# Performance work log

Hardware: AMD Instinct MI355X
Metric: run time of the kernel (lower is better)

The kernel has to match this reference:

```python
import jax, jax.numpy as jnp
import numpy as np

N_NODES = 100000
N_EDGES = 1600000
IN_CH = 128
TYPE_EMB = 32
OUT_CH = 128
N_REL = 8
N_BASES = 8
N_NTYPES = 8
FEAT = IN_CH + TYPE_EMB  # 160, RGCNConv input dim after concat


def setup_inputs() -> dict:
    key = jax.random.key(0)
    ks = jax.random.split(key, 9)
    x = jax.random.normal(ks[0], (N_NODES, IN_CH), dtype=jnp.float32)
    node_type_ids = jax.random.randint(ks[1], (N_NODES,), 0, N_NTYPES)
    edge_index = jax.random.randint(ks[2], (2, N_EDGES), 0, N_NODES)
    edge_type = jax.random.randint(ks[3], (N_EDGES,), 0, N_REL)
    emb_table = jax.random.normal(ks[4], (N_NTYPES, TYPE_EMB), dtype=jnp.float32)
    bases = jax.random.normal(ks[5], (N_BASES, FEAT, OUT_CH), dtype=jnp.float32) * (1.0 / np.sqrt(FEAT))
    comp = jax.random.normal(ks[6], (N_REL, N_BASES), dtype=jnp.float32) * (1.0 / np.sqrt(N_BASES))
    root_w = jax.random.normal(ks[7], (FEAT, OUT_CH), dtype=jnp.float32) * (1.0 / np.sqrt(FEAT))
    bias = jnp.zeros((OUT_CH,), dtype=jnp.float32)
    return {"x": x, "node_type_ids": node_type_ids, "edge_index": edge_index,
            "edge_type": edge_type, "emb_table": emb_table, "bases": bases,
            "comp": comp, "root_w": root_w, "bias": bias}


def reference(x, node_type_ids, edge_index, edge_type, emb_table, bases, comp, root_w, bias):
    N = x.shape[0]
    # node-type embedding lookup + concat
    h = jnp.concatenate([x, emb_table[node_type_ids]], axis=1)  # [N, FEAT]
    # basis decomposition: per-relation weights [R, FEAT, OUT]
    weight = jnp.einsum('rb,bio->rio', comp, bases)
    src, dst = edge_index[0], edge_index[1]
    h_src = h[src]  # [E, FEAT] -- dominant gather
    # root/self transform + bias
    out = h @ root_w + bias
    # PyG RGCNConv default aggr='mean': per-relation mean over incoming edges, summed across relations
    for r in range(weight.shape[0]):
        m = (edge_type == r).astype(h.dtype)  # [E]
        s = jax.ops.segment_sum(h_src * m[:, None], dst, num_segments=N)  # [N, FEAT]
        c = jax.ops.segment_sum(m, dst, num_segments=N)                    # [N]
        mean_r = s / jnp.maximum(c, 1.0)[:, None]
        out = out + mean_r @ weight[r]
    # dropout is identity in eval mode
    return jax.nn.relu(out)
```

## Files before the change

kernel.cpp:

```cpp
#include <hip/hip_runtime.h>

#define NN 100000
#define NE 1600000
#define INC 128
#define TE 32
#define OC 128
#define NR 8
#define NBASES 8
#define FT 160
#define KP 168
#define KW 160
#define TN 32
#define NBKT 3125
#define NCH 256
#define EPB 6250
#define CAP 896

typedef float f32x4 __attribute__((ext_vector_type(4)));
typedef float f32x2 __attribute__((ext_vector_type(2)));
typedef __bf16 bf16x8 __attribute__((ext_vector_type(8)));

__device__ __forceinline__ unsigned f2bf1(float f) {
    unsigned u = __float_as_uint(f);
    return (u + 0x7fffu + ((u >> 16) & 1u)) >> 16;
}

__device__ __forceinline__ float bflo(unsigned u) { return __uint_as_float(u << 16); }
__device__ __forceinline__ float bfhi(unsigned u) { return __uint_as_float(u & 0xFFFF0000u); }

__device__ __forceinline__ unsigned cvtpk(float a, float b) {
    unsigned r;
    asm("v_cvt_pk_bf16_f32 %0, %1, %2" : "=v"(r) : "v"(a), "v"(b));
    return r;
}

__device__ __forceinline__ int bscan_excl(int v, int* tmp) {
    int tid = threadIdx.x;
    tmp[tid] = v; __syncthreads();
#pragma unroll
    for (int d = 1; d < 256; d <<= 1) {
        int t = (tid >= d) ? tmp[tid - d] : 0;
        __syncthreads();
        tmp[tid] += t;
        __syncthreads();
    }
    return tmp[tid] - v;
}

__global__ __launch_bounds__(256) void k_prep(
    const float* __restrict__ x, const int* __restrict__ nt,
    const float* __restrict__ emb, const float* __restrict__ comp,
    const float* __restrict__ bases, const float* __restrict__ rootw,
    const int* __restrict__ ei,
    unsigned short* __restrict__ h, unsigned short* __restrict__ Wt,
    int* __restrict__ ghist, int* __restrict__ total) {
    __shared__ int hist[NBKT];
    int tid = threadIdx.x;
    int b = blockIdx.x;
    if (b < NCH) {
        for (int j = tid; j < NBKT; j += 256) hist[j] = 0;
        __syncthreads();
        int e0 = b * EPB;
#pragma unroll
        for (int kk = 0; kk < 28; kk += 4) {
            int dv[4];
#pragma unroll
            for (int u = 0; u < 4; u++) {
                int i = (kk + u) * 256 + tid;
                dv[u] = (i < EPB) ? ei[NE + e0 + i] : -1;
            }
#pragma unroll
            for (int u = 0; u < 4; u++)
                if (dv[u] >= 0) atomicAdd(&hist[dv[u] >> 5], 1);
        }
        __syncthreads();
        int* g = ghist + (size_t)b * NBKT;
        for (int j = tid; j < NBKT; j += 256) {
            int v = hist[j];
            g[j] = v;
            if (v) atomicAdd(&total[j], v);
        }
        return;
    }
    int idx = (b - NCH) * 256 + tid;
    if (idx < 9 * 128 * KW) {
        int ridx = idx / (128 * KW);
        int rem  = idx % (128 * KW);
        int o = rem / KW;
        int k = rem % KW;
        float v = 0.f;
        if (k < 128) {
            if (ridx < NR) {
#pragma unroll
                for (int bb = 0; bb < NBASES; bb++)
                    v += comp[ridx * NBASES + bb] * bases[(bb * FT + k) * OC + o];
            } else {
                v = rootw[k * OC + o];
            }
        } else if (k < 136) {
            int t = k - 128;
            if (ridx < NR) {
#pragma unroll
                for (int bb = 0; bb < NBASES; bb++) {
                    float cb = comp[ridx * NBASES + bb], s2 = 0.f;
                    for (int k2 = 0; k2 < TE; k2++)
                        s2 += emb[t * TE + k2] * bases[(bb * FT + 128 + k2) * OC + o];
                    v += cb * s2;
                }
            } else {
                for (int k2 = 0; k2 < TE; k2++)
                    v += emb[t * TE + k2] * rootw[(128 + k2) * OC + o];
            }
        }
        Wt[idx] = (unsigned short)f2bf1(v);
    }
    if (idx < NN * 16) {
        int n = idx / 16, c = idx % 16;
        const float* p = x + (size_t)n * INC + c * 8;
        f32x4 v0 = *(const f32x4*)p, v1 = *(const f32x4*)(p + 4);
        uint4 o;
        o.x = f2bf1(v0.x) | (f2bf1(v0.y) << 16);
        o.y = f2bf1(v0.z) | (f2bf1(v0.w) << 16);
        o.z = f2bf1(v1.x) | (f2bf1(v1.y) << 16);
        o.w = f2bf1(v1.z) | (f2bf1(v1.w) << 16);
        *(uint4*)(h + (size_t)n * INC + c * 8) = o;
    }
}

__global__ __launch_bounds__(256) void k_scan(const int* __restrict__ total,
                                              int* __restrict__ bstart) {
    __shared__ int tmp[256];
    int tid = threadIdx.x, s = 0, i0 = tid * 13;
    int loc[13];
#pragma unroll
    for (int i = 0; i < 13; i++) {
        int j = i0 + i;
        loc[i] = (j < NBKT) ? total[j] : 0;
        s += loc[i];
    }
    int run = bscan_excl(s, tmp);
#pragma unroll
    for (int i = 0; i < 13; i++) {
        int j = i0 + i;
        if (j < NBKT) { bstart[j] = run; run += loc[i]; }
    }
    if (tid == 0) bstart[NBKT] = NE;
}

__global__ __launch_bounds__(256) void k_off(int* __restrict__ ghist,
                                             const int* __restrict__ bstart) {
    int w = (blockIdx.x * 256 + threadIdx.x) >> 6;
    int lane = threadIdx.x & 63;
    if (w >= NBKT) return;
    size_t base = (size_t)(lane * 4) * NBKT + w;
    int v[4];
#pragma unroll
    for (int k = 0; k < 4; k++) v[k] = ghist[base + (size_t)k * NBKT];
    int s = v[0] + v[1] + v[2] + v[3];
    int inc = s;
#pragma unroll
    for (int d = 1; d < 64; d <<= 1) {
        int t = __shfl_up(inc, d, 64);
        if (lane >= d) inc += t;
    }
    int run = bstart[w] + inc - s;
#pragma unroll
    for (int k = 0; k < 4; k++) {
        ghist[base + (size_t)k * NBKT] = run;
        run += v[k];
    }
}

__global__ __launch_bounds__(256) void k_scatter(const int* __restrict__ ei, const int* __restrict__ et,
                                                 const int* __restrict__ nt,
                                                 const int* __restrict__ ghist, unsigned* __restrict__ slots) {
    __shared__ int cur[NBKT];
    int tid = threadIdx.x, b = blockIdx.x;
    for (int j = tid; j < NBKT; j += 256) cur[j] = ghist[(size_t)b * NBKT + j];
    __syncthreads();
    int e0 = b * EPB;
#pragma unroll
    for (int kk = 0; kk < 28; kk += 4) {
        int sv[4], dv[4], rv[4], tv[4];
#pragma unroll
        for (int u = 0; u < 4; u++) {
            int i = (kk + u) * 256 + tid;
            int e = e0 + ((i < EPB) ? i : 0);
            sv[u] = ei[e]; dv[u] = ei[NE + e]; rv[u] = et[e];
            if (i >= EPB) dv[u] = -1;
        }
#pragma unroll
        for (int u = 0; u < 4; u++) tv[u] = nt[sv[u]];
#pragma unroll
        for (int u = 0; u < 4; u++) {
            if (dv[u] >= 0) {
                int pos = atomicAdd(&cur[dv[u] >> 5], 1);
                slots[pos] = (unsigned)sv[u] | ((unsigned)rv[u] << 17)
                           | ((unsigned)(dv[u] & 31) << 20) | ((unsigned)tv[u] << 25);
            }
        }
    }
}

__global__ __launch_bounds__(256, 6) void k_mega(
    const unsigned short* __restrict__ h, const int* __restrict__ nt,
    const float* __restrict__ bias,
    const unsigned short* __restrict__ Wt, const int* __restrict__ bstart,
    const unsigned* __restrict__ slots, float* __restrict__ out) {
    __shared__ unsigned short featmem[2][TN * KP];
    __shared__ unsigned sl[CAP];
    __shared__ unsigned pkl[256];

    const int tid = threadIdx.x;
    const int lane = tid & 63;
    const int wave = tid >> 6;
    const int j = blockIdx.x;
    const int n0 = j * TN;

    unsigned* sl_in = reinterpret_cast<unsigned*>(&featmem[0][0]);
    int* hist = reinterpret_cast<int*>(&featmem[0][0]) + CAP;
    int* tmp  = reinterpret_cast<int*>(&featmem[0][0]) + CAP + 256;

    int s0 = bstart[j];
    int m = bstart[j + 1] - s0; if (m > CAP) m = CAP;
    for (int i = tid; i < m; i += 256) sl_in[i] = slots[s0 + i];
    hist[tid] = 0;
    __syncthreads();
    for (int i = tid; i < m; i += 256) {
        unsigned v = sl_in[i];
        atomicAdd(&hist[((v >> 17) & 7u) * 32u + ((v >> 20) & 31u)], 1);
    }
    __syncthreads();
    int v0 = hist[tid];
    int ex = bscan_excl(v0, tmp);
    pkl[tid] = (unsigned)ex | ((unsigned)v0 << 16);
    hist[tid] = ex;
    __syncthreads();
    for (int i = tid; i < m; i += 256) {
        unsigned v = sl_in[i];
        int p = atomicAdd(&hist[((v >> 17) & 7u) * 32u + ((v >> 20) & 31u)], 1);
        sl[p] = (v & 0x1FFFFu) | (((v >> 25) & 7u) << 17);
    }
    __syncthreads();

    for (int i = tid; i < TN * 20; i += 256) {
        int nl = i / 20, c = i % 20, n = n0 + nl;
        uint4 v;
        if (c < 16) {
            v = *reinterpret_cast<const uint4*>(h + (size_t)n * INC + c * 8);
        } else if (c == 16) {
            int t = nt[n];
            v.x = (t == 0 ? 0x3F80u : 0u) | (t == 1 ? 0x3F800000u : 0u);
            v.y = (t == 2 ? 0x3F80u : 0u) | (t == 3 ? 0x3F800000u : 0u);
            v.z = (t == 4 ? 0x3F80u : 0u) | (t == 5 ? 0x3F800000u : 0u);
            v.w = (t == 6 ? 0x3F80u : 0u) | (t == 7 ? 0x3F800000u : 0u);
        } else {
            v = (uint4){0u, 0u, 0u, 0u};
        }
        *reinterpret_cast<uint4*>(&featmem[0][nl * KP + c * 8]) = v;
    }

    f32x4 acc[4];
#pragma unroll
    for (int t = 0; t < 4; t++) acc[t] = (f32x4){0.f, 0.f, 0.f, 0.f};

    auto mfma_pass = [&](int ridx, const unsigned short* fm) {
        const unsigned short* fA = fm + (lane & 15) * KP + ((lane >> 4) * 8);
        const unsigned short* gB = Wt + (size_t)ridx * 128 * KW
                                   + (wave * 32 + (lane & 15)) * KW + ((lane >> 4) * 8);
#pragma unroll
        for (int kc = 0; kc < 5; kc++) {
            bf16x8 a0 = *reinterpret_cast<const bf16x8*>(fA + 0 * 16 * KP + kc * 32);
            bf16x8 a1 = *reinterpret_cast<const bf16x8*>(fA + 1 * 16 * KP + kc * 32);
#pragma unroll
            for (int ct = 0; ct < 2; ct++) {
                bf16x8 b = *reinterpret_cast<const bf16x8*>(gB + ct * 16 * KW + kc * 32);
                acc[0 * 2 + ct] = __builtin_amdgcn_mfma_f32_16x16x32_bf16(a0, b, acc[0 * 2 + ct], 0, 0, 0);
                acc[1 * 2 + ct] = __builtin_amdgcn_mfma_f32_16x16x32_bf16(a1, b, acc[1 * 2 + ct], 0, 0, 0);
            }
        }
    };

    const int g = tid >> 4, l = tid & 15;
    const unsigned* hw = reinterpret_cast<const unsigned*>(h);

    auto agg_pass = [&](int r, unsigned short* fm) {
        int b0 = r * 32 + 2 * g;
        unsigned pk0 = pkl[b0], pk1 = pkl[b0 + 1];
        int sbeg = (int)(pk0 & 0xffffu);
        int e1 = (int)(pk1 & 0xffffu);
        int send = e1 + (int)(pk1 >> 16);
        f32x2 sa[4];
#pragma unroll
        for (int i = 0; i < 4; i++) sa[i] = (f32x2){0.f, 0.f};
        f32x2 cnt2 = (f32x2){0.f, 0.f};
        float run = 0.f;
        for (int e = sbeg; e < send; e += 4) {
            uint2 wa[4], wb[4]; unsigned tpk = 0;
#pragma unroll
            for (int u = 0; u < 4; u++) {
                int eu = e + u; if (eu >= send) eu = send - 1;
                unsigned v = sl[eu];
                const unsigned* hp = hw + (size_t)(v & 0x1FFFFu) * 64 + 2 * l;
                wa[u] = *reinterpret_cast<const uint2*>(hp);
                wb[u] = *reinterpret_cast<const uint2*>(hp + 32);
                tpk |= ((v >> 17) & 7u) << (3 * u);
            }
#pragma unroll
            for (int u = 0; u < 4; u++) {
                if (e + u < send) {
                    sa[0] += (f32x2){bflo(wa[u].x), bfhi(wa[u].x)};
                    sa[1] += (f32x2){bflo(wa[u].y), bfhi(wa[u].y)};
                    sa[2] += (f32x2){bflo(wb[u].x), bfhi(wb[u].x)};
                    sa[3] += (f32x2){bflo(wb[u].y), bfhi(wb[u].y)};
                    int tt = (int)((tpk >> (3 * u)) & 7u);
                    cnt2.x += (tt == 2 * l)     ? 1.f : 0.f;
                    cnt2.y += (tt == 2 * l + 1) ? 1.f : 0.f;
                    run += 1.f;
                    int nx = e + u + 1;
                    if (nx == e1 || nx == send) {
                        int q = (e + u >= e1) ? 1 : 0;
                        float inv = __builtin_amdgcn_rcpf(run);
                        f32x2 m0 = sa[0] * inv, m1 = sa[1] * inv, m2 = sa[2] * inv,
                              m3 = sa[3] * inv, fr = cnt2 * inv;
                        unsigned* fp = reinterpret_cast<unsigned*>(fm + (2 * g + q) * KP);
                        uint2 oa, ob;
                        oa.x = cvtpk(m0.x, m0.y);
                        oa.y = cvtpk(m1.x, m1.y);
                        ob.x = cvtpk(m2.x, m2.y);
                        ob.y = cvtpk(m3.x, m3.y);
                        *reinterpret_cast<uint2*>(fp + 2 * l) = oa;
                        *reinterpret_cast<uint2*>(fp + 32 + 2 * l) = ob;
                        fp[64 + l] = cvtpk(fr.x, fr.y);
#pragma unroll
                        for (int i = 0; i < 4; i++) sa[i] = (f32x2){0.f, 0.f};
                        cnt2 = (f32x2){0.f, 0.f};
                        run = 0.f;
                    }
                }
            }
        }
#pragma unroll
        for (int q = 0; q < 2; q++) {
            if ((pkl[b0 + q] >> 16) == 0u) {
                unsigned* fp = reinterpret_cast<unsigned*>(fm + (2 * g + q) * KP);
                *reinterpret_cast<uint2*>(fp + 2 * l) = (uint2){0u, 0u};
                *reinterpret_cast<uint2*>(fp + 32 + 2 * l) = (uint2){0u, 0u};
                fp[64 + l] = 0u;
            }
        }
    };

    __syncthreads();
    int prev = 8;
    for (int r = 0; r < NR; r++) {
        agg_pass(r, &featmem[(r + 1) & 1][0]);
        mfma_pass(prev, &featmem[r & 1][0]);
        prev = r;
        __syncthreads();
    }
    mfma_pass(7, &featmem[0][0]);

    const int rq = lane >> 4;
#pragma unroll
    for (int ct = 0; ct < 2; ct++) {
        int col = wave * 32 + ct * 16 + (lane & 15);
        float bv = bias[col];
#pragma unroll
        for (int rt = 0; rt < 2; rt++) {
#pragma unroll
            for (int i = 0; i < 4; i++) {
                int n = n0 + rt * 16 + rq * 4 + i;
                float v = acc[rt * 2 + ct][i] + bv;
                out[(size_t)n * OC + col] = v > 0.f ? v : 0.f;
            }
        }
    }
}

extern "C" void kernel_launch(void* const* d_in, const int* in_sizes, int n_in,
                              void* d_out, int out_size, void* d_ws, size_t ws_size,
                              hipStream_t stream) {
    const float* x     = (const float*)d_in[0];
    const int*   ntype = (const int*)d_in[1];
    const int*   ei    = (const int*)d_in[2];
    const int*   et    = (const int*)d_in[3];
    const float* emb   = (const float*)d_in[4];
    const float* bases = (const float*)d_in[5];
    const float* comp  = (const float*)d_in[6];
    const float* rootw = (const float*)d_in[7];
    const float* bias  = (const float*)d_in[8];
    float* out = (float*)d_out;

    char* ws = (char*)d_ws;
    unsigned short* Wt     = (unsigned short*)(ws);
    unsigned short* h      = (unsigned short*)(ws + 368640);
    int*            ghist  = (int*)(ws + 25968640);
    int*            total  = (int*)(ws + 29168640);
    int*            bstart = (int*)(ws + 29181184);
    unsigned*       slots  = (unsigned*)(ws + 29193728);

    hipMemsetAsync(total, 0, NBKT * sizeof(int), stream);
    k_prep   <<<NCH + 6250, 256, 0, stream>>>(x, ntype, emb, comp, bases, rootw, ei, h, Wt, ghist, total);
    k_scan   <<<1,    256, 0, stream>>>(total, bstart);
    k_off    <<<782,  256, 0, stream>>>(ghist, bstart);
    k_scatter<<<NCH,  256, 0, stream>>>(ei, et, ntype, ghist, slots);
    k_mega   <<<NBKT, 256, 0, stream>>>(h, ntype, bias, Wt, bstart, slots, out);
}
```

Baseline: 338.6 us.

## Assign eight destination rows per wave with software-pipelined double-buffered gathers

The aggregation pass is remapped: each wave now walks 8 consecutive destination segments, and each lane handles one dword (2 bf16 features), where before 16-lane groups handled 2 segments with 4 dwords per lane. Gathers of 8 edges are double-buffered: the next batch is issued before the current one is accumulated, to hide global-load latency. The intent is fewer, wider, coalesced row loads per edge and more loads in flight. In exchange each wave runs longer serial segment chains, boundary checks against seven edges cost more, and the prefetch reads up to 16 edges past the end (clamped to the last edge).

Result: slower. 454.9 us (+34.3%).

```diff
diff --git a/kernel.cpp b/kernel.cpp
--- a/kernel.cpp
+++ b/kernel.cpp
@@ -281,72 +281,77 @@
         }
     };
 
-    const int g = tid >> 4, l = tid & 15;
     const unsigned* hw = reinterpret_cast<const unsigned*>(h);
+    const int tl2 = 2 * lane;
 
     auto agg_pass = [&](int r, unsigned short* fm) {
-        int b0 = r * 32 + 2 * g;
-        unsigned pk0 = pkl[b0], pk1 = pkl[b0 + 1];
-        int sbeg = (int)(pk0 & 0xffffu);
-        int e1 = (int)(pk1 & 0xffffu);
-        int send = e1 + (int)(pk1 >> 16);
-        f32x2 sa[4];
-#pragma unroll
-        for (int i = 0; i < 4; i++) sa[i] = (f32x2){0.f, 0.f};
-        f32x2 cnt2 = (f32x2){0.f, 0.f};
+        int b0 = r * 32 + wave * 8;
+        int sbeg = (int)(pkl[b0] & 0xffffu);
+        int e1 = (int)(pkl[b0 + 1] & 0xffffu);
+        int e2 = (int)(pkl[b0 + 2] & 0xffffu);
+        int e3 = (int)(pkl[b0 + 3] & 0xffffu);
+        int e4 = (int)(pkl[b0 + 4] & 0xffffu);
+        int e5 = (int)(pkl[b0 + 5] & 0xffffu);
+        int e6 = (int)(pkl[b0 + 6] & 0xffffu);
+        unsigned pk7 = pkl[b0 + 7];
+        int e7 = (int)(pk7 & 0xffffu);
+        int send = e7 + (int)(pk7 >> 16);
+
+        f32x2 sa = (f32x2){0.f, 0.f}, cnt2 = (f32x2){0.f, 0.f};
         float run = 0.f;
-        for (int e = sbeg; e < send; e += 4) {
-            uint2 wa[4], wb[4]; unsigned tpk = 0;
-#pragma unroll
-            for (int u = 0; u < 4; u++) {
-                int eu = e + u; if (eu >= send) eu = send - 1;
+        unsigned wA[8], wB[8]; unsigned tA = 0, tB = 0;
+
+        auto issue = [&](int eb, unsigned* w, unsigned& tp) {
+            tp = 0;
+#pragma unroll
+            for (int u = 0; u < 8; u++) {
+                int eu = eb + u; if (eu >= send) eu = send - 1;
                 unsigned v = sl[eu];
-                const unsigned* hp = hw + (size_t)(v & 0x1FFFFu) * 64 + 2 * l;
-                wa[u] = *reinterpret_cast<const uint2*>(hp);
-                wb[u] = *reinterpret_cast<const uint2*>(hp + 32);
-                tpk |= ((v >> 17) & 7u) << (3 * u);
-            }
-#pragma unroll
-            for (int u = 0; u < 4; u++) {
-                if (e + u < send) {
-                    sa[0] += (f32x2){bflo(wa[u].x), bfhi(wa[u].x)};
-                    sa[1] += (f32x2){bflo(wa[u].y), bfhi(wa[u].y)};
-                    sa[2] += (f32x2){bflo(wb[u].x), bfhi(wb[u].x)};
-                    sa[3] += (f32x2){bflo(wb[u].y), bfhi(wb[u].y)};
-                    int tt = (int)((tpk >> (3 * u)) & 7u);
-                    cnt2.x += (tt == 2 * l)     ? 1.f : 0.f;
-                    cnt2.y += (tt == 2 * l + 1) ? 1.f : 0.f;
+                w[u] = hw[(size_t)(v & 0x1FFFFu) * 64 + lane];
+                tp |= ((v >> 17) & 7u) << (3 * u);
+            }
+        };
+        auto consume = [&](int eb, const unsigned* w, unsigned tp) {
+#pragma unroll
+            for (int u = 0; u < 8; u++) {
+                int p = eb + u;
+                if (p < send) {
+                    unsigned dw = w[u];
+                    sa += (f32x2){bflo(dw), bfhi(dw)};
+                    int tt = (int)((tp >> (3 * u)) & 7u);
+                    cnt2.x += (tt == tl2)     ? 1.f : 0.f;
+                    cnt2.y += (tt == tl2 + 1) ? 1.f : 0.f;
                     run += 1.f;
-                    int nx = e + u + 1;
-                    if (nx == e1 || nx == send) {
-                        int q = (e + u >= e1) ? 1 : 0;
+                    int nx = p + 1;
+                    if (nx == e1 || nx == e2 || nx == e3 || nx == e4 ||
+                        nx == e5 || nx == e6 || nx == e7 || nx == send) {
+                        int q = (p >= e1) + (p >= e2) + (p >= e3) + (p >= e4)
+                              + (p >= e5) + (p >= e6) + (p >= e7);
                         float inv = __builtin_amdgcn_rcpf(run);
-                        f32x2 m0 = sa[0] * inv, m1 = sa[1] * inv, m2 = sa[2] * inv,
-                              m3 = sa[3] * inv, fr = cnt2 * inv;
-                        unsigned* fp = reinterpret_cast<unsigned*>(fm + (2 * g + q) * KP);
-                        uint2 oa, ob;
-                        oa.x = cvtpk(m0.x, m0.y);
-                        oa.y = cvtpk(m1.x, m1.y);
-                        ob.x = cvtpk(m2.x, m2.y);
-                        ob.y = cvtpk(m3.x, m3.y);
-                        *reinterpret_cast<uint2*>(fp + 2 * l) = oa;
-                        *reinterpret_cast<uint2*>(fp + 32 + 2 * l) = ob;
-                        fp[64 + l] = cvtpk(fr.x, fr.y);
-#pragma unroll
-                        for (int i = 0; i < 4; i++) sa[i] = (f32x2){0.f, 0.f};
-                        cnt2 = (f32x2){0.f, 0.f};
-                        run = 0.f;
+                        unsigned* fp = reinterpret_cast<unsigned*>(fm + (wave * 8 + q) * KP);
+                        fp[lane] = cvtpk(sa.x * inv, sa.y * inv);
+                        if (lane < 16) fp[64 + lane] = cvtpk(cnt2.x * inv, cnt2.y * inv);
+                        sa = (f32x2){0.f, 0.f}; cnt2 = (f32x2){0.f, 0.f}; run = 0.f;
                     }
                 }
             }
-        }
-#pragma unroll
-        for (int q = 0; q < 2; q++) {
+        };
+
+        if (sbeg < send) {
+            issue(sbeg, wA, tA);
+            for (int e = sbeg; e < send; e += 16) {
+                issue(e + 8, wB, tB);
+                consume(e, wA, tA);
+                issue(e + 16, wA, tA);
+                consume(e + 8, wB, tB);
+            }
+        }
+#pragma unroll
+        for (int q = 0; q < 8; q++) {
             if ((pkl[b0 + q] >> 16) == 0u) {
-                unsigned* fp = reinterpret_cast<unsigned*>(fm + (2 * g + q) * KP);
-                *reinterpret_cast<uint2*>(fp + 2 * l) = (uint2){0u, 0u};
-                *reinterpret_cast<uint2*>(fp + 32 + 2 * l) = (uint2){0u, 0u};
-                fp[64 + l] = 0u;
+                unsigned* fp = reinterpret_cast<unsigned*>(fm + (wave * 8 + q) * KP);
+                fp[lane] = 0u;
+                if (lane < 16) fp[64 + lane] = 0u;
             }
         }
     };
```

## Fuse bucket scan and offset kernels into one grid-barrier kernel

Applied to the files above, without the earlier changes.

Replaces the single-block k_scan and the k_off kernel with one persistent kernel, k_sso. It computes the per-bucket totals from ghist, crosses a software grid barrier, has every block redundantly scan the totals in shared memory, then writes the per-chunk offsets. This removes the global atomicAdd into total inside k_prep, one kernel launch and the single-block serial scan stage. In exchange it adds a spin-wait grid barrier that assumes all 256 blocks are resident at once, and every block repeats the scan.

After: 393.9 us. 1.16x slower.

```diff
diff --git a/kernel.cpp b/kernel.cpp
--- a/kernel.cpp
+++ b/kernel.cpp
@@ -47,13 +47,28 @@
     return tmp[tid] - v;
 }
 
+__device__ __forceinline__ void gridbar(int* bar, int nblk) {
+    __syncthreads();
+    if (threadIdx.x == 0) {
+        int g = __hip_atomic_load(bar + 1, __ATOMIC_RELAXED, __HIP_MEMORY_SCOPE_AGENT);
+        if (__hip_atomic_fetch_add(bar, 1, __ATOMIC_ACQ_REL, __HIP_MEMORY_SCOPE_AGENT) == nblk - 1) {
+            __hip_atomic_store(bar, 0, __ATOMIC_RELAXED, __HIP_MEMORY_SCOPE_AGENT);
+            __hip_atomic_fetch_add(bar + 1, 1, __ATOMIC_ACQ_REL, __HIP_MEMORY_SCOPE_AGENT);
+        } else {
+            while (__hip_atomic_load(bar + 1, __ATOMIC_ACQUIRE, __HIP_MEMORY_SCOPE_AGENT) == g)
+                __builtin_amdgcn_s_sleep(1);
+        }
+    }
+    __syncthreads();
+}
+
 __global__ __launch_bounds__(256) void k_prep(
     const float* __restrict__ x, const int* __restrict__ nt,
     const float* __restrict__ emb, const float* __restrict__ comp,
     const float* __restrict__ bases, const float* __restrict__ rootw,
     const int* __restrict__ ei,
     unsigned short* __restrict__ h, unsigned short* __restrict__ Wt,
-    int* __restrict__ ghist, int* __restrict__ total) {
+    int* __restrict__ ghist) {
     __shared__ int hist[NBKT];
     int tid = threadIdx.x;
     int b = blockIdx.x;
@@ -75,11 +90,7 @@
         }
         __syncthreads();
         int* g = ghist + (size_t)b * NBKT;
-        for (int j = tid; j < NBKT; j += 256) {
-            int v = hist[j];
-            g[j] = v;
-            if (v) atomicAdd(&total[j], v);
-        }
+        for (int j = tid; j < NBKT; j += 256) g[j] = hist[j];
         return;
     }
     int idx = (b - NCH) * 256 + tid;
@@ -127,47 +138,66 @@
     }
 }
 
-__global__ __launch_bounds__(256) void k_scan(const int* __restrict__ total,
-                                              int* __restrict__ bstart) {
+__global__ __launch_bounds__(256) void k_sso(int* __restrict__ ghist, int* __restrict__ total,
+                                             int* __restrict__ bstart, int* __restrict__ bar) {
+    __shared__ int tot[NBKT];
     __shared__ int tmp[256];
-    int tid = threadIdx.x, s = 0, i0 = tid * 13;
+    int tid = threadIdx.x;
+    int lane = tid & 63;
+    int wid0 = blockIdx.x * 4 + (tid >> 6);
+
+    for (int j = wid0; j < NBKT; j += 1024) {
+        size_t base = (size_t)(lane * 4) * NBKT + j;
+        int s = 0;
+#pragma unroll
+        for (int k = 0; k < 4; k++) s += ghist[base + (size_t)k * NBKT];
+#pragma unroll
+        for (int d = 32; d > 0; d >>= 1) s += __shfl_xor(s, d, 64);
+        if (lane == 0) total[j] = s;
+    }
+    __threadfence();
+    gridbar(bar, 256);
+
+    for (int j = tid; j < NBKT; j += 256) tot[j] = total[j];
+    __syncthreads();
+    int i0 = tid * 13, s2 = 0;
     int loc[13];
 #pragma unroll
     for (int i = 0; i < 13; i++) {
         int j = i0 + i;
-        loc[i] = (j < NBKT) ? total[j] : 0;
-        s += loc[i];
-    }
-    int run = bscan_excl(s, tmp);
+        loc[i] = (j < NBKT) ? tot[j] : 0;
+        s2 += loc[i];
+    }
+    int run = bscan_excl(s2, tmp);
 #pragma unroll
     for (int i = 0; i < 13; i++) {
         int j = i0 + i;
-        if (j < NBKT) { bstart[j] = run; run += loc[i]; }
-    }
-    if (tid == 0) bstart[NBKT] = NE;
-}
-
-__global__ __launch_bounds__(256) void k_off(int* __restrict__ ghist,
-                                             const int* __restrict__ bstart) {
-    int w = (blockIdx.x * 256 + threadIdx.x) >> 6;
-    int lane = threadIdx.x & 63;
-    if (w >= NBKT) return;
-    size_t base = (size_t)(lane * 4) * NBKT + w;
-    int v[4];
-#pragma unroll
-    for (int k = 0; k < 4; k++) v[k] = ghist[base + (size_t)k * NBKT];
-    int s = v[0] + v[1] + v[2] + v[3];
-    int inc = s;
-#pragma unroll
-    for (int d = 1; d < 64; d <<= 1) {
-        int t = __shfl_up(inc, d, 64);
-        if (lane >= d) inc += t;
-    }
-    int run = bstart[w] + inc - s;
-#pragma unroll
-    for (int k = 0; k < 4; k++) {
-        ghist[base + (size_t)k * NBKT] = run;
-        run += v[k];
+        if (j < NBKT) { tot[j] = run; run += loc[i]; }
+    }
+    __syncthreads();
+    if (blockIdx.x == 0) {
+        for (int j = tid; j < NBKT; j += 256) bstart[j] = tot[j];
+        if (tid == 0) bstart[NBKT] = NE;
+    }
+
+    for (int j = wid0; j < NBKT; j += 1024) {
+        size_t base = (size_t)(lane * 4) * NBKT + j;
+        int v[4];
+#pragma unroll
+        for (int k = 0; k < 4; k++) v[k] = ghist[base + (size_t)k * NBKT];
+        int s = v[0] + v[1] + v[2] + v[3];
+        int inc = s;
+#pragma unroll
+        for (int d = 1; d < 64; d <<= 1) {
+            int t = __shfl_up(inc, d, 64);
+            if (lane >= d) inc += t;
+        }
+        int run2 = tot[j] + inc - s;
+#pragma unroll
+        for (int k = 0; k < 4; k++) {
+            ghist[base + (size_t)k * NBKT] = run2;
+            run2 += v[k];
+        }
     }
 }
 
@@ -398,12 +428,12 @@
     int*            ghist  = (int*)(ws + 25968640);
     int*            total  = (int*)(ws + 29168640);
     int*            bstart = (int*)(ws + 29181184);
-    unsigned*       slots  = (unsigned*)(ws + 29193728);
-
-    hipMemsetAsync(total, 0, NBKT * sizeof(int), stream);
-    k_prep   <<<NCH + 6250, 256, 0, stream>>>(x, ntype, emb, comp, bases, rootw, ei, h, Wt, ghist, total);
-    k_scan   <<<1,    256, 0, stream>>>(total, bstart);
-    k_off    <<<782,  256, 0, stream>>>(ghist, bstart);
+    int*            bar    = (int*)(ws + 29193728);
+    unsigned*       slots  = (unsigned*)(ws + 29193984);
+
+    hipMemsetAsync(bar, 0, 8, stream);
+    k_prep   <<<NCH + 6250, 256, 0, stream>>>(x, ntype, emb, comp, bases, rootw, ei, h, Wt, ghist);
+    k_sso    <<<256,  256, 0, stream>>>(ghist, total, bstart, bar);
     k_scatter<<<NCH,  256, 0, stream>>>(ei, et, ntype, ghist, slots);
     k_mega   <<<NBKT, 256, 0, stream>>>(h, ntype, bias, Wt, bstart, slots, out);
 }
```
